# Optimization experiments

Hardware: AMD Instinct MI355X
Metric: run time of the kernel (lower is better)

Reference implementation:

```python
import jax, jax.numpy as jnp
import numpy as np
import math

D_MODEL = 512
N_HEAD = 8
D_HEAD = 64
N_LAYER = 12
D_FF = 2048
EMB_SIZES = [32, 128, 256, 256, 32, 64]
N_TOKEN = [32, 32, 90, 70, 8, 8]
EPS_ATTN = 1e-6
EPS_LN = 1e-5


def _pos_encoding(seq, d):
    pos = np.arange(seq, dtype=np.float32)[:, None]
    div = np.exp(np.arange(0, d, 2, dtype=np.float32) * (-math.log(10000.0) / d))
    pe = np.zeros((seq, d), np.float32)
    pe[:, 0::2] = np.sin(pos * div)
    pe[:, 1::2] = np.cos(pos * div)
    return jnp.asarray(pe)


def _layernorm(x, g, b):
    mu = jnp.mean(x, axis=-1, keepdims=True)
    var = jnp.var(x, axis=-1, keepdims=True)
    return (x - mu) * jax.lax.rsqrt(var + EPS_LN) * g + b


def _phi(x):
    # elu(x) + 1
    return jnp.where(x > 0, x + 1.0, jnp.exp(x))


def _causal_linear_attention(h, wq, bq, wk, bk, wv, bv, wo, bo):
    B, S, _ = h.shape
    q = _phi((h @ wq + bq).reshape(B, S, N_HEAD, D_HEAD))
    k = _phi((h @ wk + bk).reshape(B, S, N_HEAD, D_HEAD))
    v = (h @ wv + bv).reshape(B, S, N_HEAD, D_HEAD)
    # cumulative K^T V state: [B,S,H,D,D]
    kv = jnp.cumsum(k[..., :, None] * v[..., None, :], axis=1)
    ksum = jnp.cumsum(k, axis=1)
    z = 1.0 / (jnp.einsum('bshd,bshd->bsh', q, ksum) + EPS_ATTN)
    out = jnp.einsum('bshd,bshde->bshe', q, kv) * z[..., None]
    return out.reshape(B, S, D_MODEL) @ wo + bo


def _forward(x, emb_bar, emb_position, emb_pitch, emb_duration, emb_type, emb_emotion,
             in_w, in_b, wq, bq, wk, bk, wv, bv, wo, bo,
             ln1_g, ln1_b, w1, b1, w2, b2, ln2_g, ln2_b,
             lnf_g, lnf_b, proj_emo_w, proj_emo_b):
    tables = [emb_bar, emb_position, emb_pitch, emb_duration, emb_type, emb_emotion]
    embs = jnp.concatenate(
        [jnp.take(t, x[..., i], axis=0) * math.sqrt(EMB_SIZES[i]) for i, t in enumerate(tables)],
        axis=-1)  # [B,S,768]
    h = embs @ in_w + in_b
    S = h.shape[1]
    h = h + _pos_encoding(S, D_MODEL)[None, :, :]  # dropout is identity in eval

    def layer(hc, p):
        (wq_, bq_, wk_, bk_, wv_, bv_, wo_, bo_,
         g1, be1, w1_, b1_, w2_, b2_, g2, be2) = p
        hc = hc + _causal_linear_attention(hc, wq_, bq_, wk_, bk_, wv_, bv_, wo_, bo_)
        hc = _layernorm(hc, g1, be1)
        y = jax.nn.gelu(hc @ w1_ + b1_, approximate=False) @ w2_ + b2_
        hc = _layernorm(hc + y, g2, be2)
        return hc, None

    params = (wq, bq, wk, bk, wv, bv, wo, bo, ln1_g, ln1_b, w1, b1, w2, b2, ln2_g, ln2_b)
    h, _ = jax.lax.scan(layer, h, params)
    h = _layernorm(h, lnf_g, lnf_b)  # final encoder norm
    y_emotion = h @ proj_emo_w + proj_emo_b
    return h, y_emotion


def setup_inputs() -> dict:
    key = jax.random.key(0)
    ks = jax.random.split(key, 16)
    B, S = 1, 1024
    x = jax.random.randint(ks[0], (B, S, 6), 0, 8)

    def lin(k, fin, fout):
        k1, k2 = jax.random.split(k)
        lim = 1.0 / np.sqrt(fin)
        return (jax.random.uniform(k1, (fin, fout), minval=-lim, maxval=lim),
                jax.random.uniform(k2, (fout,), minval=-lim, maxval=lim))

    def stack_lin(k, fin, fout):
        kk = jax.random.split(k, N_LAYER)
        ws, bs = zip(*[lin(kk[i], fin, fout) for i in range(N_LAYER)])
        return jnp.stack(ws), jnp.stack(bs)

    def stack_ln(val):
        return jnp.full((N_LAYER, D_MODEL), val, jnp.float32)

    inp = {'x': x}
    names = ['emb_bar', 'emb_position', 'emb_pitch', 'emb_duration', 'emb_type', 'emb_emotion']
    for i, n in enumerate(names):
        inp[n] = jax.random.normal(jax.random.fold_in(ks[1], i), (N_TOKEN[i], EMB_SIZES[i])) * 0.02
    inp['in_w'], inp['in_b'] = lin(ks[2], sum(EMB_SIZES), D_MODEL)
    inp['wq'], inp['bq'] = stack_lin(ks[3], D_MODEL, D_MODEL)
    inp['wk'], inp['bk'] = stack_lin(ks[4], D_MODEL, D_MODEL)
    inp['wv'], inp['bv'] = stack_lin(ks[5], D_MODEL, D_MODEL)
    inp['wo'], inp['bo'] = stack_lin(ks[6], D_MODEL, D_MODEL)
    inp['ln1_g'], inp['ln1_b'] = stack_ln(1.0), stack_ln(0.0)
    inp['w1'], inp['b1'] = stack_lin(ks[7], D_MODEL, D_FF)
    inp['w2'], inp['b2'] = stack_lin(ks[8], D_FF, D_MODEL)
    inp['ln2_g'], inp['ln2_b'] = stack_ln(1.0), stack_ln(0.0)
    inp['lnf_g'], inp['lnf_b'] = jnp.ones((D_MODEL,)), jnp.zeros((D_MODEL,))
    inp['proj_emo_w'], inp['proj_emo_b'] = lin(ks[9], D_MODEL, N_TOKEN[5])
    return inp


def reference(x, emb_bar, emb_position, emb_pitch, emb_duration, emb_type, emb_emotion,
              in_w, in_b, wq, bq, wk, bk, wv, bv, wo, bo,
              ln1_g, ln1_b, w1, b1, w2, b2, ln2_g, ln2_b,
              lnf_g, lnf_b, proj_emo_w, proj_emo_b):
    return _forward(x, emb_bar, emb_position, emb_pitch, emb_duration, emb_type, emb_emotion,
                    in_w, in_b, wq, bq, wk, bk, wv, bv, wo, bo,
                    ln1_g, ln1_b, w1, b1, w2, b2, ln2_g, ln2_b,
                    lnf_g, lnf_b, proj_emo_w, proj_emo_b)
```

## Files before the change

### kernel.cpp

```cpp
#include <hip/hip_runtime.h>
#include <hip/hip_bf16.h>
#include <math.h>


#define S_LEN 1024
#define DM 512
#define NH 8
#define DH 64
#define DFF 2048
#define NLAYER 12
#define CHUNK 64
#define NCH (S_LEN / CHUNK)

#define ACT_NONE 0
#define ACT_PHI  1
#define ACT_GELU 2

typedef short s16x8 __attribute__((ext_vector_type(8)));
typedef float f32x4 __attribute__((ext_vector_type(4)));

__device__ __forceinline__ short f2bf(float x) {
    __hip_bfloat16 h = __float2bfloat16(x);
    return *reinterpret_cast<short*>(&h);
}

__device__ __forceinline__ void fma4(f32x4& a, float s, const f32x4 v) {
    a.x = fmaf(s, v.x, a.x); a.y = fmaf(s, v.y, a.y);
    a.z = fmaf(s, v.z, a.z); a.w = fmaf(s, v.w, a.w);
}

__device__ __forceinline__ void tile_barrier() {
    asm volatile("s_waitcnt lgkmcnt(0)" ::: "memory");
    __builtin_amdgcn_s_barrier();
    asm volatile("" ::: "memory");
}

__global__ __launch_bounds__(256) void embed_kernel(
    const int* __restrict__ x,
    const float* __restrict__ t0, const float* __restrict__ t1,
    const float* __restrict__ t2, const float* __restrict__ t3,
    const float* __restrict__ t4, const float* __restrict__ t5,
    short* __restrict__ EMBb)
{
    int s = blockIdx.x;
    __shared__ int xi[6];
    if (threadIdx.x < 6) xi[threadIdx.x] = x[s * 6 + threadIdx.x];
    __syncthreads();
    for (int j = threadIdx.x; j < 768; j += 256) {
        int i, off, width; const float* t; float sc;
        if (j < 32)       { i = 0; off = 0;   t = t0; sc = 5.656854249f;  width = 32;  }
        else if (j < 160) { i = 1; off = 32;  t = t1; sc = 11.3137085f;   width = 128; }
        else if (j < 416) { i = 2; off = 160; t = t2; sc = 16.0f;         width = 256; }
        else if (j < 672) { i = 3; off = 416; t = t3; sc = 16.0f;         width = 256; }
        else if (j < 704) { i = 4; off = 672; t = t4; sc = 5.656854249f;  width = 32;  }
        else              { i = 5; off = 704; t = t5; sc = 8.0f;          width = 64;  }
        EMBb[s * 768 + j] = f2bf(t[xi[i] * width + (j - off)] * sc);
    }
}

__global__ __launch_bounds__(256) void transpose_w(
    const float* __restrict__ in, short* __restrict__ out, int K, int N)
{
    __shared__ short t[64][66];
    const int b = blockIdx.z;
    const int n0 = blockIdx.x * 64, k0 = blockIdx.y * 64;
    const float* ip = in + (size_t)b * K * N;
    short* op = out + (size_t)b * K * N;
    const int c = threadIdx.x & 63, r0 = (threadIdx.x >> 6) * 16;
    #pragma unroll
    for (int i = 0; i < 16; ++i)
        t[c][r0 + i] = f2bf(ip[(size_t)(k0 + r0 + i) * N + n0 + c]);
    __syncthreads();
    #pragma unroll
    for (int i = 0; i < 16; ++i)
        op[(size_t)(n0 + r0 + i) * K + k0 + c] = t[r0 + i][c];
}

__global__ __launch_bounds__(256) void transpose4_w(
    const float* __restrict__ wA, const float* __restrict__ wB,
    const float* __restrict__ wC, const float* __restrict__ wD,
    short* __restrict__ oA, short* __restrict__ oB,
    short* __restrict__ oC, short* __restrict__ oD)
{
    __shared__ short t[64][66];
    const int zz = blockIdx.z;
    const int which = zz & 3, b = zz >> 2;
    const float* in = (which == 0) ? wA : (which == 1) ? wB : (which == 2) ? wC : wD;
    short* out      = (which == 0) ? oA : (which == 1) ? oB : (which == 2) ? oC : oD;
    const int n0 = blockIdx.x * 64, k0 = blockIdx.y * 64;
    const float* ip = in + (size_t)b * DM * DM;
    short* op = out + (size_t)b * DM * DM;
    const int c = threadIdx.x & 63, r0 = (threadIdx.x >> 6) * 16;
    #pragma unroll
    for (int i = 0; i < 16; ++i)
        t[c][r0 + i] = f2bf(ip[(size_t)(k0 + r0 + i) * DM + n0 + c]);
    __syncthreads();
    #pragma unroll
    for (int i = 0; i < 16; ++i)
        op[(size_t)(n0 + r0 + i) * DM + k0 + c] = t[r0 + i][c];
}

__device__ __forceinline__ float apply_act(float v, int act) {
    if (act == ACT_PHI)       return (v > 0.0f) ? (v + 1.0f) : expf(v);
    else if (act == ACT_GELU) return 0.5f * v * (1.0f + erff(v * 0.70710678118654752f));
    return v;
}


__device__ __forceinline__ void ldswr64(short* lds, int srow, int scolb,
                                        const s16x8 r[2])
{
    const int bc = scolb ^ ((srow & 7) << 4);
    #pragma unroll
    for (int p = 0; p < 2; ++p)
        *(s16x8*)((char*)lds + (p * 32 + srow) * 128 + bc) = r[p];
}

__device__ __forceinline__ void compute64(
    const short* __restrict__ As, const short* __restrict__ Bs,
    int wr, int wc, int l15, int q, f32x4 acc[2][2])
{
    #pragma unroll
    for (int kh = 0; kh < 2; ++kh) {
        const int kb = kh * 64 + q * 16;
        s16x8 a[2], b[2];
        #pragma unroll
        for (int m = 0; m < 2; ++m) {
            int row = wr * 32 + m * 16 + l15;
            a[m] = *(const s16x8*)((const char*)As + row * 128 + (kb ^ ((row & 7) << 4)));
        }
        #pragma unroll
        for (int n = 0; n < 2; ++n) {
            int row = wc * 32 + n * 16 + l15;
            b[n] = *(const s16x8*)((const char*)Bs + row * 128 + (kb ^ ((row & 7) << 4)));
        }
        #pragma unroll
        for (int m = 0; m < 2; ++m)
            #pragma unroll
            for (int n = 0; n < 2; ++n)
                acc[m][n] = __builtin_amdgcn_mfma_f32_16x16x32_bf16(
                    a[m], b[n], acc[m][n], 0, 0, 0);
    }
}

__global__ __launch_bounds__(256) void gemm64(
    const short* __restrict__ A, const short* __restrict__ BT,
    const float* __restrict__ bias, const float* __restrict__ resid,
    float* __restrict__ Cf, short* __restrict__ Cbf,
    int N, int K, int act, int add_pe, int zparts)
{
    __shared__ short As[2][4096];
    __shared__ short Bs[2][4096];
    const int tid = threadIdx.x;
    const int row0 = blockIdx.y * 64, col0 = blockIdx.x * 64;
    const int z = blockIdx.z;
    const int Kz = K / zparts;
    const int kbase = z * Kz;
    const int w = tid >> 6, lane = tid & 63, q = lane >> 4, l15 = lane & 15;
    const int wr = w >> 1, wc = w & 1;
    const int nt = Kz >> 6;

    const int srow = tid >> 3;
    const int scolb = (tid & 7) * 16;
    const char* gA = (const char*)(A  + (size_t)(row0 + srow) * K + kbase) + scolb;
    const char* gB = (const char*)(BT + (size_t)(col0 + srow) * K + kbase) + scolb;
    const size_t rstep = (size_t)32 * K * 2;

    s16x8 ra[2], rb[2];
    #pragma unroll
    for (int p = 0; p < 2; ++p) {
        ra[p] = *(const s16x8*)(gA + p * rstep);
        rb[p] = *(const s16x8*)(gB + p * rstep);
    }
    ldswr64(As[0], srow, scolb, ra);
    ldswr64(Bs[0], srow, scolb, rb);
    if (nt > 1) {
        #pragma unroll
        for (int p = 0; p < 2; ++p) {
            ra[p] = *(const s16x8*)(gA + p * rstep + 128);
            rb[p] = *(const s16x8*)(gB + p * rstep + 128);
        }
    }
    tile_barrier();

    f32x4 acc[2][2] = {};
    int cur = 0;
    for (int t = 0; t < nt; ++t) {
        compute64(As[cur], Bs[cur], wr, wc, l15, q, acc);
        if (t + 1 < nt) {
            ldswr64(As[cur ^ 1], srow, scolb, ra);
            ldswr64(Bs[cur ^ 1], srow, scolb, rb);
            if (t + 2 < nt) {
                size_t ko = (size_t)(t + 2) * 128;
                #pragma unroll
                for (int p = 0; p < 2; ++p) {
                    ra[p] = *(const s16x8*)(gA + p * rstep + ko);
                    rb[p] = *(const s16x8*)(gB + p * rstep + ko);
                }
            }
            tile_barrier();
        }
        cur ^= 1;
    }

    if (zparts > 1 && Cf) Cf += (size_t)z * S_LEN * N;

    const int rbase = row0 + wr * 32 + q * 4;
    const int cbase = col0 + wc * 32 + l15;
    #pragma unroll
    for (int n = 0; n < 2; ++n) {
        int c = cbase + n * 16;
        float bia = (z == 0) ? bias[c] : 0.0f;
        #pragma unroll
        for (int m = 0; m < 2; ++m) {
            #pragma unroll
            for (int rg = 0; rg < 4; ++rg) {
                int r = rbase + m * 16 + rg;
                float v = apply_act(acc[m][n][rg] + bia, act);
                if (resid) v += resid[(size_t)r * N + c];
                if (add_pe) {
                    float freq = expf((float)(c & ~1) * (-9.210340371976184f / 512.0f));
                    float ang = (float)r * freq;
                    v += (c & 1) ? cosf(ang) : sinf(ang);
                }
                if (Cf)  Cf[(size_t)r * N + c] = v;
                if (Cbf) Cbf[(size_t)r * N + c] = f2bf(v);
            }
        }
    }
}

__global__ __launch_bounds__(256) void qkv64(
    const short* __restrict__ Hb,
    const short* __restrict__ qT, const short* __restrict__ kT, const short* __restrict__ vT,
    const float* __restrict__ bq, const float* __restrict__ bk, const float* __restrict__ bv,
    float* __restrict__ Qb, float* __restrict__ Kb, float* __restrict__ Vb)
{
    __shared__ short As[2][4096];
    __shared__ short Bs[2][4096];
    const int sel  = blockIdx.x >> 3;
    const int col0 = (blockIdx.x & 7) * 64;
    const int row0 = blockIdx.y * 64;
    const short* BT   = (sel == 0) ? qT : (sel == 1) ? kT : vT;
    const float* bias = (sel == 0) ? bq : (sel == 1) ? bk : bv;
    float* C          = (sel == 0) ? Qb : (sel == 1) ? Kb : Vb;
    const bool phi = (sel < 2);

    const int tid = threadIdx.x;
    const int w = tid >> 6, lane = tid & 63, q = lane >> 4, l15 = lane & 15;
    const int wr = w >> 1, wc = w & 1;

    const int srow = tid >> 3;
    const int scolb = (tid & 7) * 16;
    const char* gA = (const char*)(Hb + (size_t)(row0 + srow) * DM) + scolb;
    const char* gB = (const char*)(BT + (size_t)(col0 + srow) * DM) + scolb;
    const size_t rstep = (size_t)32 * DM * 2;

    s16x8 ra[2], rb[2];
    #pragma unroll
    for (int p = 0; p < 2; ++p) {
        ra[p] = *(const s16x8*)(gA + p * rstep);
        rb[p] = *(const s16x8*)(gB + p * rstep);
    }
    ldswr64(As[0], srow, scolb, ra);
    ldswr64(Bs[0], srow, scolb, rb);
    #pragma unroll
    for (int p = 0; p < 2; ++p) {
        ra[p] = *(const s16x8*)(gA + p * rstep + 128);
        rb[p] = *(const s16x8*)(gB + p * rstep + 128);
    }
    tile_barrier();

    f32x4 acc[2][2] = {};
    int cur = 0;
    for (int t = 0; t < 8; ++t) {
        compute64(As[cur], Bs[cur], wr, wc, l15, q, acc);
        if (t + 1 < 8) {
            ldswr64(As[cur ^ 1], srow, scolb, ra);
            ldswr64(Bs[cur ^ 1], srow, scolb, rb);
            if (t + 2 < 8) {
                size_t ko = (size_t)(t + 2) * 128;
                #pragma unroll
                for (int p = 0; p < 2; ++p) {
                    ra[p] = *(const s16x8*)(gA + p * rstep + ko);
                    rb[p] = *(const s16x8*)(gB + p * rstep + ko);
                }
            }
            tile_barrier();
        }
        cur ^= 1;
    }

    const int rbase = row0 + wr * 32 + q * 4;
    const int cbase = col0 + wc * 32 + l15;
    #pragma unroll
    for (int n = 0; n < 2; ++n) {
        int c = cbase + n * 16;
        float bia = bias[c];
        #pragma unroll
        for (int m = 0; m < 2; ++m) {
            #pragma unroll
            for (int rg = 0; rg < 4; ++rg) {
                int r = rbase + m * 16 + rg;
                float v = acc[m][n][rg] + bia;
                if (phi) v = (v > 0.0f) ? (v + 1.0f) : expf(v);
                C[(size_t)r * DM + c] = v;
            }
        }
    }
}

__global__ __launch_bounds__(256) void chunk_stats_kernel(
    const float* __restrict__ Kb, const float* __restrict__ Vb,
    float* __restrict__ KVC, float* __restrict__ KSC)
{
    const int h = blockIdx.x >> 4, c = blockIdx.x & 15;
    const int tid = threadIdx.x;
    __shared__ float Ks[64][68];
    __shared__ float Vs[64][68];
    #pragma unroll
    for (int it = 0; it < 4; ++it) {
        int j = tid + it * 256;
        int r = j >> 4, d0 = (j & 15) * 4;
        size_t g = (size_t)(c * CHUNK + r) * DM + h * 64 + d0;
        *(f32x4*)(&Ks[r][d0]) = *(const f32x4*)(Kb + g);
        *(f32x4*)(&Vs[r][d0]) = *(const f32x4*)(Vb + g);
    }
    __syncthreads();
    const int di = (tid >> 4) * 4, ei = (tid & 15) * 4;
    f32x4 a0 = {}, a1 = {}, a2 = {}, a3 = {}, ks = {};
    #pragma unroll 8
    for (int t = 0; t < 64; ++t) {
        f32x4 kk = *(const f32x4*)(&Ks[t][di]);
        f32x4 vv = *(const f32x4*)(&Vs[t][ei]);
        fma4(a0, kk.x, vv); fma4(a1, kk.y, vv);
        fma4(a2, kk.z, vv); fma4(a3, kk.w, vv);
        ks += kk;
    }
    float* out = KVC + (size_t)(c * NH + h) * 4096;
    *(f32x4*)(out + (size_t)(di + 0) * 64 + ei) = a0;
    *(f32x4*)(out + (size_t)(di + 1) * 64 + ei) = a1;
    *(f32x4*)(out + (size_t)(di + 2) * 64 + ei) = a2;
    *(f32x4*)(out + (size_t)(di + 3) * 64 + ei) = a3;
    if ((tid & 15) == 0)
        *(f32x4*)(KSC + (size_t)(c * NH + h) * 64 + di) = ks;
}

__global__ __launch_bounds__(256) void attn_out_kernel(
    const float* __restrict__ Qb, const float* __restrict__ Kb,
    const float* __restrict__ Vb, const float* __restrict__ KVC,
    const float* __restrict__ KSC, short* __restrict__ Ab)
{
    const int h = blockIdx.x >> 4, c = blockIdx.x & 15;
    const int tid = threadIdx.x;
    __shared__ float Qt[64][68];
    __shared__ float Kt[64][68];
    __shared__ float Vs[64][68];
    __shared__ float Ms[64][68];
    __shared__ float St[64][68];
    __shared__ float KSs[64];

    {
        f32x4 macc[4] = {};
        for (int cp = 0; cp < c; ++cp) {
            const float* src = KVC + (size_t)(cp * NH + h) * 4096;
            #pragma unroll
            for (int it = 0; it < 4; ++it)
                macc[it] += *(const f32x4*)(src + (size_t)(tid + it * 256) * 4);
        }
        #pragma unroll
        for (int it = 0; it < 4; ++it) {
            int j = tid + it * 256;
            *(f32x4*)(&Ms[j >> 4][(j & 15) * 4]) = macc[it];
        }
        if (tid < 64) {
            float s = 0.0f;
            for (int cp = 0; cp < c; ++cp)
                s += KSC[(size_t)(cp * NH + h) * 64 + tid];
            KSs[tid] = s;
        }
    }
    #pragma unroll
    for (int it = 0; it < 4; ++it) {
        int j = tid + it * 256;
        int r = j >> 4, d0 = (j & 15) * 4;
        size_t g = (size_t)(c * CHUNK + r) * DM + h * 64 + d0;
        f32x4 q = *(const f32x4*)(Qb + g);
        f32x4 k = *(const f32x4*)(Kb + g);
        f32x4 v = *(const f32x4*)(Vb + g);
        Qt[d0 + 0][r] = q.x; Qt[d0 + 1][r] = q.y; Qt[d0 + 2][r] = q.z; Qt[d0 + 3][r] = q.w;
        Kt[d0 + 0][r] = k.x; Kt[d0 + 1][r] = k.y; Kt[d0 + 2][r] = k.z; Kt[d0 + 3][r] = k.w;
        *(f32x4*)(&Vs[r][d0]) = v;
    }
    __syncthreads();

    const int si = tid >> 4, ti = tid & 15;
    const int s0 = si * 4, t0 = ti * 4;

    f32x4 accO0 = {}, accO1 = {}, accO2 = {}, accO3 = {};
    f32x4 den = {};
    #pragma unroll 8
    for (int d = 0; d < 64; ++d) {
        f32x4 qv = *(const f32x4*)(&Qt[d][s0]);
        f32x4 mv = *(const f32x4*)(&Ms[d][t0]);
        float ks = KSs[d];
        fma4(accO0, qv.x, mv); fma4(accO1, qv.y, mv);
        fma4(accO2, qv.z, mv); fma4(accO3, qv.w, mv);
        fma4(den, ks, qv);
    }

    f32x4 p0 = {}, p1 = {}, p2 = {}, p3 = {};
    if (ti <= si) {
        #pragma unroll 8
        for (int d = 0; d < 64; ++d) {
            f32x4 qv = *(const f32x4*)(&Qt[d][s0]);
            f32x4 kv = *(const f32x4*)(&Kt[d][t0]);
            fma4(p0, qv.x, kv); fma4(p1, qv.y, kv);
            fma4(p2, qv.z, kv); fma4(p3, qv.w, kv);
        }
        if (ti == si) {
            p0.y = 0.0f; p0.z = 0.0f; p0.w = 0.0f;
            p1.z = 0.0f; p1.w = 0.0f;
            p2.w = 0.0f;
        }
    }
    St[t0 + 0][s0 + 0] = p0.x; St[t0 + 1][s0 + 0] = p0.y;
    St[t0 + 2][s0 + 0] = p0.z; St[t0 + 3][s0 + 0] = p0.w;
    St[t0 + 0][s0 + 1] = p1.x; St[t0 + 1][s0 + 1] = p1.y;
    St[t0 + 2][s0 + 1] = p1.z; St[t0 + 3][s0 + 1] = p1.w;
    St[t0 + 0][s0 + 2] = p2.x; St[t0 + 1][s0 + 2] = p2.y;
    St[t0 + 2][s0 + 2] = p2.z; St[t0 + 3][s0 + 2] = p2.w;
    St[t0 + 0][s0 + 3] = p3.x; St[t0 + 1][s0 + 3] = p3.y;
    St[t0 + 2][s0 + 3] = p3.z; St[t0 + 3][s0 + 3] = p3.w;
    __syncthreads();

    const int tmax = s0 + 4;
    #pragma unroll 4
    for (int t2 = 0; t2 < tmax; ++t2) {
        f32x4 sv = *(const f32x4*)(&St[t2][s0]);
        f32x4 vv = *(const f32x4*)(&Vs[t2][t0]);
        fma4(accO0, sv.x, vv); fma4(accO1, sv.y, vv);
        fma4(accO2, sv.z, vv); fma4(accO3, sv.w, vv);
        den += sv;
    }

    short* op = Ab + (size_t)(c * CHUNK + s0) * DM + h * 64 + t0;
    {
        float z = 1.0f / (den.x + 1e-6f);
        short4 o; o.x = f2bf(accO0.x * z); o.y = f2bf(accO0.y * z);
        o.z = f2bf(accO0.z * z); o.w = f2bf(accO0.w * z);
        *reinterpret_cast<short4*>(op) = o;
    }
    {
        float z = 1.0f / (den.y + 1e-6f);
        short4 o; o.x = f2bf(accO1.x * z); o.y = f2bf(accO1.y * z);
        o.z = f2bf(accO1.z * z); o.w = f2bf(accO1.w * z);
        *reinterpret_cast<short4*>(op + DM) = o;
    }
    {
        float z = 1.0f / (den.z + 1e-6f);
        short4 o; o.x = f2bf(accO2.x * z); o.y = f2bf(accO2.y * z);
        o.z = f2bf(accO2.z * z); o.w = f2bf(accO2.w * z);
        *reinterpret_cast<short4*>(op + 2 * DM) = o;
    }
    {
        float z = 1.0f / (den.w + 1e-6f);
        short4 o; o.x = f2bf(accO3.x * z); o.y = f2bf(accO3.y * z);
        o.z = f2bf(accO3.z * z); o.w = f2bf(accO3.w * z);
        *reinterpret_cast<short4*>(op + 3 * DM) = o;
    }
}

__global__ __launch_bounds__(64) void ln_kernel64(
    const float* __restrict__ X, const float* __restrict__ X2,
    const float* __restrict__ resid,
    const float* __restrict__ g, const float* __restrict__ b,
    float* __restrict__ O, short* __restrict__ Ob)
{
    const int row = blockIdx.x;
    const size_t base = (size_t)row * DM;
    const int t = threadIdx.x;
    const int i0 = 4 * t, i1 = 256 + 4 * t;
    f32x4 v0 = *(const f32x4*)(X + base + i0);
    f32x4 v1 = *(const f32x4*)(X + base + i1);
    if (X2) {
        v0 += *(const f32x4*)(X2 + base + i0);
        v1 += *(const f32x4*)(X2 + base + i1);
    }
    if (resid) {
        v0 += *(const f32x4*)(resid + base + i0);
        v1 += *(const f32x4*)(resid + base + i1);
    }
    float s = v0.x + v0.y + v0.z + v0.w + v1.x + v1.y + v1.z + v1.w;
    #pragma unroll
    for (int m = 1; m < 64; m <<= 1) s += __shfl_xor(s, m, 64);
    float mean = s * (1.0f / 512.0f);
    f32x4 d0 = v0 - mean, d1 = v1 - mean;
    float ss = d0.x * d0.x + d0.y * d0.y + d0.z * d0.z + d0.w * d0.w
             + d1.x * d1.x + d1.y * d1.y + d1.z * d1.z + d1.w * d1.w;
    #pragma unroll
    for (int m = 1; m < 64; m <<= 1) ss += __shfl_xor(ss, m, 64);
    float var = ss * (1.0f / 512.0f);
    float rs = 1.0f / sqrtf(var + 1e-5f);
    f32x4 g0 = *(const f32x4*)(g + i0), g1v = *(const f32x4*)(g + i1);
    f32x4 b0 = *(const f32x4*)(b + i0), b1v = *(const f32x4*)(b + i1);
    f32x4 o0 = d0 * rs * g0 + b0;
    f32x4 o1 = d1 * rs * g1v + b1v;
    *(f32x4*)(O + base + i0) = o0;
    *(f32x4*)(O + base + i1) = o1;
    if (Ob) {
        short4 s0; s0.x = f2bf(o0.x); s0.y = f2bf(o0.y); s0.z = f2bf(o0.z); s0.w = f2bf(o0.w);
        short4 s1; s1.x = f2bf(o1.x); s1.y = f2bf(o1.y); s1.z = f2bf(o1.z); s1.w = f2bf(o1.w);
        *reinterpret_cast<short4*>(Ob + base + i0) = s0;
        *reinterpret_cast<short4*>(Ob + base + i1) = s1;
    }
}

__global__ __launch_bounds__(256) void proj_emo_kernel(
    const float* __restrict__ HF, const float* __restrict__ pw,
    const float* __restrict__ pb, float* __restrict__ out)
{
    __shared__ float pws[4096];
    for (int i = threadIdx.x; i < 4096; i += 256) pws[i] = pw[i];
    __syncthreads();
    int idx = blockIdx.x * 256 + threadIdx.x;
    int r = idx >> 3, e = idx & 7;
    float acc = pb[e];
    const float* h = HF + (size_t)r * DM;
    for (int d = 0; d < DM; d += 4) {
        f32x4 hv = *(const f32x4*)(h + d);
        acc += hv.x * pws[(d + 0) * 8 + e] + hv.y * pws[(d + 1) * 8 + e]
             + hv.z * pws[(d + 2) * 8 + e] + hv.w * pws[(d + 3) * 8 + e];
    }
    out[idx] = acc;
}

extern "C" void kernel_launch(void* const* d_in, const int* in_sizes, int n_in,
                              void* d_out, int out_size, void* d_ws, size_t ws_size,
                              hipStream_t stream)
{
    const int*   x    = (const int*)d_in[0];
    const float* e0   = (const float*)d_in[1];
    const float* e1   = (const float*)d_in[2];
    const float* e2   = (const float*)d_in[3];
    const float* e3   = (const float*)d_in[4];
    const float* e4   = (const float*)d_in[5];
    const float* e5   = (const float*)d_in[6];
    const float* in_w = (const float*)d_in[7];
    const float* in_b = (const float*)d_in[8];
    const float* wq   = (const float*)d_in[9];
    const float* bq   = (const float*)d_in[10];
    const float* wk   = (const float*)d_in[11];
    const float* bk   = (const float*)d_in[12];
    const float* wv   = (const float*)d_in[13];
    const float* bv   = (const float*)d_in[14];
    const float* wo   = (const float*)d_in[15];
    const float* bo   = (const float*)d_in[16];
    const float* g1   = (const float*)d_in[17];
    const float* be1  = (const float*)d_in[18];
    const float* w1   = (const float*)d_in[19];
    const float* b1   = (const float*)d_in[20];
    const float* w2   = (const float*)d_in[21];
    const float* b2   = (const float*)d_in[22];
    const float* g2   = (const float*)d_in[23];
    const float* be2  = (const float*)d_in[24];
    const float* gf   = (const float*)d_in[25];
    const float* bfin = (const float*)d_in[26];
    const float* pw   = (const float*)d_in[27];
    const float* pb   = (const float*)d_in[28];
    float* outp = (float*)d_out;

    float* ws = (float*)d_ws;
    float* H    = ws;
    float* Y    = ws + 524288;
    float* Y2   = ws + 1048576;
    float* Qb   = ws + 1572864;
    float* Kb   = ws + 2097152;
    float* Vb   = ws + 2621440;
    float* KVC  = ws + 3145728;
    float* KSC  = ws + 3670016;
    short* sb   = (short*)(ws + 3678208);
    short* Hb   = sb;
    short* Ab   = sb + 524288;
    short* FFb  = sb + 1048576;
    short* EMBb = FFb;
    short* inT  = sb + 3145728;
    short* qT   = inT + 393216;
    short* kT   = qT + 3145728;
    short* vT   = kT + 3145728;
    short* oT   = vT + 3145728;
    short* w1T  = oT + 3145728;
    short* w2T  = w1T + 12582912;

    const dim3 blk256(256), blk64(64);

    transpose_w<<<dim3(8, 12, 1),  blk256, 0, stream>>>(in_w, inT, 768, DM);
    transpose4_w<<<dim3(8, 8, 48), blk256, 0, stream>>>(wq, wk, wv, wo,
                                                        qT, kT, vT, oT);
    transpose_w<<<dim3(32, 8, 12), blk256, 0, stream>>>(w1, w1T, DM, DFF);
    transpose_w<<<dim3(8, 32, 12), blk256, 0, stream>>>(w2, w2T, DFF, DM);

    embed_kernel<<<S_LEN, blk256, 0, stream>>>(x, e0, e1, e2, e3, e4, e5, EMBb);
    gemm64<<<dim3(8, 16, 1), blk256, 0, stream>>>(EMBb, inT, in_b, nullptr,
                                                  H, Hb, DM, 768, ACT_NONE, 1, 1);

    for (int l = 0; l < NLAYER; ++l) {
        const short* qT_l = qT + (size_t)l * DM * DM;
        const short* kT_l = kT + (size_t)l * DM * DM;
        const short* vT_l = vT + (size_t)l * DM * DM;
        const short* oT_l = oT + (size_t)l * DM * DM;
        const short* w1T_l = w1T + (size_t)l * DM * DFF;
        const short* w2T_l = w2T + (size_t)l * DM * DFF;
        const float* bq_l = bq + l * DM;  const float* bk_l = bk + l * DM;
        const float* bv_l = bv + l * DM;  const float* bo_l = bo + l * DM;
        const float* b1_l = b1 + l * DFF; const float* b2_l = b2 + l * DM;

        qkv64<<<dim3(24, 16), blk256, 0, stream>>>(Hb, qT_l, kT_l, vT_l,
                                                   bq_l, bk_l, bv_l, Qb, Kb, Vb);

        chunk_stats_kernel<<<NCH * NH, blk256, 0, stream>>>(Kb, Vb, KVC, KSC);
        attn_out_kernel<<<NCH * NH, blk256, 0, stream>>>(Qb, Kb, Vb, KVC, KSC, Ab);

        gemm64<<<dim3(8, 16, 2), blk256, 0, stream>>>(Ab, oT_l, bo_l, nullptr,
                                                      Y, nullptr, DM, DM, ACT_NONE, 0, 2);
        ln_kernel64<<<S_LEN, blk64, 0, stream>>>(Y, Y2, H,
                                                 g1 + l * DM, be1 + l * DM, H, Hb);

        gemm64<<<dim3(32, 16, 1), blk256, 0, stream>>>(Hb, w1T_l, b1_l, nullptr,
                                                       nullptr, FFb, DFF, DM, ACT_GELU, 0, 1);
        gemm64<<<dim3(8, 16, 2), blk256, 0, stream>>>(FFb, w2T_l, b2_l, nullptr,
                                                      Y, nullptr, DM, DFF, ACT_NONE, 0, 2);
        ln_kernel64<<<S_LEN, blk64, 0, stream>>>(Y, Y2, H,
                                                 g2 + l * DM, be2 + l * DM, H, Hb);
    }

    ln_kernel64<<<S_LEN, blk64, 0, stream>>>(H, nullptr, nullptr, gf, bfin, outp, nullptr);
    proj_emo_kernel<<<8192 / 256, blk256, 0, stream>>>(outp, pw, pb, outp + 524288);
}
```

Baseline: 1.049 ms.

## Fuse per-chunk KV stats into QKV GEMM and LN with emotion projection

The QKV projection kernel now has K/V blocks compute both K and V tiles for the same head and chunk, then reduce them in shared memory into the per-chunk K^T V and K-sum statistics. This removes the separate chunk_stats kernel launch and its global reload of K and V. The final layernorm is also merged with the 8-wide emotion projection. The cost is that K/V blocks use more LDS (48KB) and registers, which may lower occupancy, and the grid is uneven because Q blocks do half the work of K/V blocks.

```diff
diff --git a/kernel.cpp b/kernel.cpp
--- a/kernel.cpp
+++ b/kernel.cpp
@@ -140,6 +140,39 @@
             for (int n = 0; n < 2; ++n)
                 acc[m][n] = __builtin_amdgcn_mfma_f32_16x16x32_bf16(
                     a[m], b[n], acc[m][n], 0, 0, 0);
+    }
+}
+
+__device__ __forceinline__ void compute64x2(
+    const short* __restrict__ As, const short* __restrict__ Bs0,
+    const short* __restrict__ Bs1,
+    int wr, int wc, int l15, int q, f32x4 acc0[2][2], f32x4 acc1[2][2])
+{
+    #pragma unroll
+    for (int kh = 0; kh < 2; ++kh) {
+        const int kb = kh * 64 + q * 16;
+        s16x8 a[2], b0[2], b1[2];
+        #pragma unroll
+        for (int m = 0; m < 2; ++m) {
+            int row = wr * 32 + m * 16 + l15;
+            a[m] = *(const s16x8*)((const char*)As + row * 128 + (kb ^ ((row & 7) << 4)));
+        }
+        #pragma unroll
+        for (int n = 0; n < 2; ++n) {
+            int row = wc * 32 + n * 16 + l15;
+            int off = row * 128 + (kb ^ ((row & 7) << 4));
+            b0[n] = *(const s16x8*)((const char*)Bs0 + off);
+            b1[n] = *(const s16x8*)((const char*)Bs1 + off);
+        }
+        #pragma unroll
+        for (int m = 0; m < 2; ++m)
+            #pragma unroll
+            for (int n = 0; n < 2; ++n) {
+                acc0[m][n] = __builtin_amdgcn_mfma_f32_16x16x32_bf16(
+                    a[m], b0[n], acc0[m][n], 0, 0, 0);
+                acc1[m][n] = __builtin_amdgcn_mfma_f32_16x16x32_bf16(
+                    a[m], b1[n], acc1[m][n], 0, 0, 0);
+            }
     }
 }
 
@@ -230,60 +263,124 @@
     }
 }
 
-__global__ __launch_bounds__(256) void qkv64(
+__global__ __launch_bounds__(256) void qkv_fused(
     const short* __restrict__ Hb,
     const short* __restrict__ qT, const short* __restrict__ kT, const short* __restrict__ vT,
     const float* __restrict__ bq, const float* __restrict__ bk, const float* __restrict__ bv,
-    float* __restrict__ Qb, float* __restrict__ Kb, float* __restrict__ Vb)
-{
-    __shared__ short As[2][4096];
-    __shared__ short Bs[2][4096];
-    const int sel  = blockIdx.x >> 3;
-    const int col0 = (blockIdx.x & 7) * 64;
+    float* __restrict__ Qb, float* __restrict__ Kb, float* __restrict__ Vb,
+    float* __restrict__ KVC, float* __restrict__ KSC)
+{
+    __shared__ char smem[49152];
+    short* As  = (short*)smem;
+    short* Bs0 = (short*)(smem + 16384);
+    short* Bs1 = (short*)(smem + 32768);
+
+    const int tid = threadIdx.x;
+    const bool isKV = blockIdx.x >= 8;
+    const int colb = blockIdx.x & 7;
+    const int col0 = colb * 64;
     const int row0 = blockIdx.y * 64;
-    const short* BT   = (sel == 0) ? qT : (sel == 1) ? kT : vT;
-    const float* bias = (sel == 0) ? bq : (sel == 1) ? bk : bv;
-    float* C          = (sel == 0) ? Qb : (sel == 1) ? Kb : Vb;
-    const bool phi = (sel < 2);
-
-    const int tid = threadIdx.x;
     const int w = tid >> 6, lane = tid & 63, q = lane >> 4, l15 = lane & 15;
     const int wr = w >> 1, wc = w & 1;
 
     const int srow = tid >> 3;
     const int scolb = (tid & 7) * 16;
     const char* gA = (const char*)(Hb + (size_t)(row0 + srow) * DM) + scolb;
-    const char* gB = (const char*)(BT + (size_t)(col0 + srow) * DM) + scolb;
     const size_t rstep = (size_t)32 * DM * 2;
 
-    s16x8 ra[2], rb[2];
+    if (!isKV) {
+        const char* gB = (const char*)(qT + (size_t)(col0 + srow) * DM) + scolb;
+        s16x8 ra[2], rb[2];
+        #pragma unroll
+        for (int p = 0; p < 2; ++p) {
+            ra[p] = *(const s16x8*)(gA + p * rstep);
+            rb[p] = *(const s16x8*)(gB + p * rstep);
+        }
+        ldswr64(As, srow, scolb, ra);
+        ldswr64(Bs0, srow, scolb, rb);
+        #pragma unroll
+        for (int p = 0; p < 2; ++p) {
+            ra[p] = *(const s16x8*)(gA + p * rstep + 128);
+            rb[p] = *(const s16x8*)(gB + p * rstep + 128);
+        }
+        tile_barrier();
+
+        f32x4 acc[2][2] = {};
+        int cur = 0;
+        for (int t = 0; t < 8; ++t) {
+            compute64(As + cur * 4096, Bs0 + cur * 4096, wr, wc, l15, q, acc);
+            if (t + 1 < 8) {
+                ldswr64(As + (cur ^ 1) * 4096, srow, scolb, ra);
+                ldswr64(Bs0 + (cur ^ 1) * 4096, srow, scolb, rb);
+                if (t + 2 < 8) {
+                    size_t ko = (size_t)(t + 2) * 128;
+                    #pragma unroll
+                    for (int p = 0; p < 2; ++p) {
+                        ra[p] = *(const s16x8*)(gA + p * rstep + ko);
+                        rb[p] = *(const s16x8*)(gB + p * rstep + ko);
+                    }
+                }
+                tile_barrier();
+            }
+            cur ^= 1;
+        }
+
+        const int rbase = row0 + wr * 32 + q * 4;
+        const int cbase = col0 + wc * 32 + l15;
+        #pragma unroll
+        for (int n = 0; n < 2; ++n) {
+            int c = cbase + n * 16;
+            float bia = bq[c];
+            #pragma unroll
+            for (int m = 0; m < 2; ++m) {
+                #pragma unroll
+                for (int rg = 0; rg < 4; ++rg) {
+                    int r = rbase + m * 16 + rg;
+                    float v = acc[m][n][rg] + bia;
+                    v = (v > 0.0f) ? (v + 1.0f) : expf(v);
+                    Qb[(size_t)r * DM + c] = v;
+                }
+            }
+        }
+        return;
+    }
+
+    const char* gBk = (const char*)(kT + (size_t)(col0 + srow) * DM) + scolb;
+    const char* gBv = (const char*)(vT + (size_t)(col0 + srow) * DM) + scolb;
+    s16x8 ra[2], rbk[2], rbv[2];
     #pragma unroll
     for (int p = 0; p < 2; ++p) {
-        ra[p] = *(const s16x8*)(gA + p * rstep);
-        rb[p] = *(const s16x8*)(gB + p * rstep);
-    }
-    ldswr64(As[0], srow, scolb, ra);
-    ldswr64(Bs[0], srow, scolb, rb);
+        ra[p]  = *(const s16x8*)(gA + p * rstep);
+        rbk[p] = *(const s16x8*)(gBk + p * rstep);
+        rbv[p] = *(const s16x8*)(gBv + p * rstep);
+    }
+    ldswr64(As, srow, scolb, ra);
+    ldswr64(Bs0, srow, scolb, rbk);
+    ldswr64(Bs1, srow, scolb, rbv);
     #pragma unroll
     for (int p = 0; p < 2; ++p) {
-        ra[p] = *(const s16x8*)(gA + p * rstep + 128);
-        rb[p] = *(const s16x8*)(gB + p * rstep + 128);
+        ra[p]  = *(const s16x8*)(gA + p * rstep + 128);
+        rbk[p] = *(const s16x8*)(gBk + p * rstep + 128);
+        rbv[p] = *(const s16x8*)(gBv + p * rstep + 128);
     }
     tile_barrier();
 
-    f32x4 acc[2][2] = {};
+    f32x4 acck[2][2] = {}, accv[2][2] = {};
     int cur = 0;
     for (int t = 0; t < 8; ++t) {
-        compute64(As[cur], Bs[cur], wr, wc, l15, q, acc);
+        compute64x2(As + cur * 4096, Bs0 + cur * 4096, Bs1 + cur * 4096,
+                    wr, wc, l15, q, acck, accv);
         if (t + 1 < 8) {
-            ldswr64(As[cur ^ 1], srow, scolb, ra);
-            ldswr64(Bs[cur ^ 1], srow, scolb, rb);
+            ldswr64(As + (cur ^ 1) * 4096, srow, scolb, ra);
+            ldswr64(Bs0 + (cur ^ 1) * 4096, srow, scolb, rbk);
+            ldswr64(Bs1 + (cur ^ 1) * 4096, srow, scolb, rbv);
             if (t + 2 < 8) {
                 size_t ko = (size_t)(t + 2) * 128;
                 #pragma unroll
                 for (int p = 0; p < 2; ++p) {
-                    ra[p] = *(const s16x8*)(gA + p * rstep + ko);
-                    rb[p] = *(const s16x8*)(gB + p * rstep + ko);
+                    ra[p]  = *(const s16x8*)(gA + p * rstep + ko);
+                    rbk[p] = *(const s16x8*)(gBk + p * rstep + ko);
+                    rbv[p] = *(const s16x8*)(gBv + p * rstep + ko);
                 }
             }
             tile_barrier();
@@ -291,48 +388,43 @@
         cur ^= 1;
     }
 
-    const int rbase = row0 + wr * 32 + q * 4;
-    const int cbase = col0 + wc * 32 + l15;
-    #pragma unroll
-    for (int n = 0; n < 2; ++n) {
-        int c = cbase + n * 16;
-        float bia = bias[c];
-        #pragma unroll
-        for (int m = 0; m < 2; ++m) {
+    __syncthreads();
+    float* Ksf = (float*)smem;
+    float* Vsf = (float*)(smem + 17408);
+    {
+        const int lrb = wr * 32 + q * 4;
+        const int lcb = wc * 32 + l15;
+        #pragma unroll
+        for (int n = 0; n < 2; ++n) {
+            int lc = lcb + n * 16;
+            int c = col0 + lc;
+            float bk_ = bk[c], bv_ = bv[c];
             #pragma unroll
-            for (int rg = 0; rg < 4; ++rg) {
-                int r = rbase + m * 16 + rg;
-                float v = acc[m][n][rg] + bia;
-                if (phi) v = (v > 0.0f) ? (v + 1.0f) : expf(v);
-                C[(size_t)r * DM + c] = v;
+            for (int m = 0; m < 2; ++m) {
+                #pragma unroll
+                for (int rg = 0; rg < 4; ++rg) {
+                    int lr = lrb + m * 16 + rg;
+                    int r = row0 + lr;
+                    float kv = acck[m][n][rg] + bk_;
+                    kv = (kv > 0.0f) ? (kv + 1.0f) : expf(kv);
+                    float vv = accv[m][n][rg] + bv_;
+                    Kb[(size_t)r * DM + c] = kv;
+                    Vb[(size_t)r * DM + c] = vv;
+                    Ksf[lr * 68 + lc] = kv;
+                    Vsf[lr * 68 + lc] = vv;
+                }
             }
         }
     }
-}
-
-__global__ __launch_bounds__(256) void chunk_stats_kernel(
-    const float* __restrict__ Kb, const float* __restrict__ Vb,
-    float* __restrict__ KVC, float* __restrict__ KSC)
-{
-    const int h = blockIdx.x >> 4, c = blockIdx.x & 15;
-    const int tid = threadIdx.x;
-    __shared__ float Ks[64][68];
-    __shared__ float Vs[64][68];
-    #pragma unroll
-    for (int it = 0; it < 4; ++it) {
-        int j = tid + it * 256;
-        int r = j >> 4, d0 = (j & 15) * 4;
-        size_t g = (size_t)(c * CHUNK + r) * DM + h * 64 + d0;
-        *(f32x4*)(&Ks[r][d0]) = *(const f32x4*)(Kb + g);
-        *(f32x4*)(&Vs[r][d0]) = *(const f32x4*)(Vb + g);
-    }
     __syncthreads();
+
+    const int c = blockIdx.y, h = colb;
     const int di = (tid >> 4) * 4, ei = (tid & 15) * 4;
     f32x4 a0 = {}, a1 = {}, a2 = {}, a3 = {}, ks = {};
     #pragma unroll 8
     for (int t = 0; t < 64; ++t) {
-        f32x4 kk = *(const f32x4*)(&Ks[t][di]);
-        f32x4 vv = *(const f32x4*)(&Vs[t][ei]);
+        f32x4 kk = *(const f32x4*)(Ksf + t * 68 + di);
+        f32x4 vv = *(const f32x4*)(Vsf + t * 68 + ei);
         fma4(a0, kk.x, vv); fma4(a1, kk.y, vv);
         fma4(a2, kk.z, vv); fma4(a3, kk.w, vv);
         ks += kk;
@@ -516,23 +608,49 @@
     }
 }
 
-__global__ __launch_bounds__(256) void proj_emo_kernel(
-    const float* __restrict__ HF, const float* __restrict__ pw,
-    const float* __restrict__ pb, float* __restrict__ out)
-{
-    __shared__ float pws[4096];
-    for (int i = threadIdx.x; i < 4096; i += 256) pws[i] = pw[i];
+__global__ __launch_bounds__(64) void ln_final_proj(
+    const float* __restrict__ X,
+    const float* __restrict__ g, const float* __restrict__ b,
+    const float* __restrict__ pw, const float* __restrict__ pb,
+    float* __restrict__ Hout, float* __restrict__ Eout)
+{
+    __shared__ float hrow[512];
+    const int row = blockIdx.x;
+    const size_t base = (size_t)row * DM;
+    const int t = threadIdx.x;
+    const int i0 = 4 * t, i1 = 256 + 4 * t;
+    f32x4 v0 = *(const f32x4*)(X + base + i0);
+    f32x4 v1 = *(const f32x4*)(X + base + i1);
+    float s = v0.x + v0.y + v0.z + v0.w + v1.x + v1.y + v1.z + v1.w;
+    #pragma unroll
+    for (int m = 1; m < 64; m <<= 1) s += __shfl_xor(s, m, 64);
+    float mean = s * (1.0f / 512.0f);
+    f32x4 d0 = v0 - mean, d1 = v1 - mean;
+    float ss = d0.x * d0.x + d0.y * d0.y + d0.z * d0.z + d0.w * d0.w
+             + d1.x * d1.x + d1.y * d1.y + d1.z * d1.z + d1.w * d1.w;
+    #pragma unroll
+    for (int m = 1; m < 64; m <<= 1) ss += __shfl_xor(ss, m, 64);
+    float var = ss * (1.0f / 512.0f);
+    float rs = 1.0f / sqrtf(var + 1e-5f);
+    f32x4 g0 = *(const f32x4*)(g + i0), g1v = *(const f32x4*)(g + i1);
+    f32x4 b0 = *(const f32x4*)(b + i0), b1v = *(const f32x4*)(b + i1);
+    f32x4 o0 = d0 * rs * g0 + b0;
+    f32x4 o1 = d1 * rs * g1v + b1v;
+    *(f32x4*)(Hout + base + i0) = o0;
+    *(f32x4*)(Hout + base + i1) = o1;
+    *(f32x4*)(&hrow[i0]) = o0;
+    *(f32x4*)(&hrow[i1]) = o1;
     __syncthreads();
-    int idx = blockIdx.x * 256 + threadIdx.x;
-    int r = idx >> 3, e = idx & 7;
-    float acc = pb[e];
-    const float* h = HF + (size_t)r * DM;
-    for (int d = 0; d < DM; d += 4) {
-        f32x4 hv = *(const f32x4*)(h + d);
-        acc += hv.x * pws[(d + 0) * 8 + e] + hv.y * pws[(d + 1) * 8 + e]
-             + hv.z * pws[(d + 2) * 8 + e] + hv.w * pws[(d + 3) * 8 + e];
-    }
-    out[idx] = acc;
+
+    const int e = t & 7, seg = t >> 3;
+    float acc = 0.0f;
+    #pragma unroll 16
+    for (int d = seg * 64; d < seg * 64 + 64; ++d)
+        acc = fmaf(hrow[d], pw[d * 8 + e], acc);
+    acc += __shfl_xor(acc, 8, 64);
+    acc += __shfl_xor(acc, 16, 64);
+    acc += __shfl_xor(acc, 32, 64);
+    if (t < 8) Eout[(size_t)row * 8 + t] = acc + pb[t];
 }
 
 extern "C" void kernel_launch(void* const* d_in, const int* in_sizes, int n_in,
@@ -615,10 +733,10 @@
         const float* bv_l = bv + l * DM;  const float* bo_l = bo + l * DM;
         const float* b1_l = b1 + l * DFF; const float* b2_l = b2 + l * DM;
 
-        qkv64<<<dim3(24, 16), blk256, 0, stream>>>(Hb, qT_l, kT_l, vT_l,
-                                                   bq_l, bk_l, bv_l, Qb, Kb, Vb);
-
-        chunk_stats_kernel<<<NCH * NH, blk256, 0, stream>>>(Kb, Vb, KVC, KSC);
+        qkv_fused<<<dim3(16, 16), blk256, 0, stream>>>(Hb, qT_l, kT_l, vT_l,
+                                                       bq_l, bk_l, bv_l,
+                                                       Qb, Kb, Vb, KVC, KSC);
+
         attn_out_kernel<<<NCH * NH, blk256, 0, stream>>>(Qb, Kb, Vb, KVC, KSC, Ab);
 
         gemm64<<<dim3(8, 16, 2), blk256, 0, stream>>>(Ab, oT_l, bo_l, nullptr,
@@ -634,6 +752,6 @@
                                                  g2 + l * DM, be2 + l * DM, H, Hb);
     }
 
-    ln_kernel64<<<S_LEN, blk64, 0, stream>>>(H, nullptr, nullptr, gf, bfin, outp, nullptr);
-    proj_emo_kernel<<<8192 / 256, blk256, 0, stream>>>(outp, pw, pb, outp + 524288);
-}
+    ln_final_proj<<<S_LEN, blk64, 0, stream>>>(H, gf, bfin, pw, pb,
+                                               outp, outp + 524288);
+}
```

Result: faster. 1.015 ms (-3.2%).
